# Kernel optimization log

Hardware: AMD Instinct MI355X
Metric: run time of the kernel (lower is better)

Reference implementation:

```python
import jax, jax.numpy as jnp
import numpy as np

# Layered-DAG regularization of the dynamic active_path graph.
H, N, BATCH, D, R = 6, 16, 32, 512, 64   # hop levels, nodes/level, batch, dim, low-rank
M = (H - 1) * N                           # nodes with weights (levels 1..H-1)
ETA_W = 0.015
LAM_C, LAM_R = 0.65, 0.35
THETA0 = 0.5
SPEC_MIN, SPEC_MAX = 0.3, 4.0
BETA1, BETA2, EPS = 0.9, 0.999, 1e-8
W_MAX = float(np.sqrt(D) * 2.0)
DW_CLIP = 5.0


def _spectral_norm(A1, B1):
    # largest singular value of W = A1 @ B1.T via power iteration using only low-rank products
    d = A1.shape[0]
    def body(_, u):
        w = A1 @ (B1.T @ (B1 @ (A1.T @ u)))  # (W W^T) u
        return w / (jnp.linalg.norm(w) + 1e-12)
    u0 = jnp.ones((d,), A1.dtype) / jnp.sqrt(jnp.asarray(d, A1.dtype))
    u = jax.lax.fori_loop(0, 20, body, u0)
    return jnp.linalg.norm(B1 @ (A1.T @ u))


def _update_node(A1, B1, mA, vA, mB, vB, Vin, T_local):
    # dual-signal (contrastive + retrograde) weight update, Adam step t=1, is_positive=True
    W = A1 @ B1.T                       # (D, D)
    Vw = Vin @ W.T                      # (BATCH, D) pre-activation (record.V_weighted)
    Vout = jnp.tanh(Vw)                 # record.V_out (tanh primitive)
    fprime = 1.0 - Vout ** 2            # primitive_derivative for tanh
    goodness = (Vout ** 2).sum(-1).mean()
    theta = THETA0 * ((Vin ** 2).sum(-1).mean() + 1e-9)   # goodness_scale_input=True
    delta = goodness - theta
    Vout_grad = (Vout * fprime * delta).mean(0)
    Vin_mean = Vin.mean(0)
    dW_c = jnp.outer(Vout_grad, Vin_mean)
    dW_r = jnp.outer(T_local.mean(0) * fprime.mean(0), Vin_mean)
    dW = LAM_C * dW_c + LAM_R * dW_r
    gnorm = jnp.linalg.norm(dW)
    dW = dW * jnp.where(gnorm > DW_CLIP, DW_CLIP / (gnorm + 1e-12), 1.0)
    gA = dW @ B1
    gB = dW.T @ A1
    mA_n = BETA1 * mA + (1 - BETA1) * gA
    vA_n = BETA2 * vA + (1 - BETA2) * gA ** 2
    A_new = A1 - ETA_W * (mA_n / (1 - BETA1)) / (jnp.sqrt(vA_n / (1 - BETA2)) + EPS)
    mB_n = BETA1 * mB + (1 - BETA1) * gB
    vB_n = BETA2 * vB + (1 - BETA2) * gB ** 2
    B_new = B1 - ETA_W * (mB_n / (1 - BETA1)) / (jnp.sqrt(vB_n / (1 - BETA2)) + EPS)
    return jnp.clip(A_new, -W_MAX, W_MAX), jnp.clip(B_new, -W_MAX, W_MAX)


def _forward(Y_hat, Y_star, V_edges, A, Bw, m_A, v_A, m_B, v_B):
    T_v = (Y_star - Y_hat) / jnp.sqrt(jnp.asarray(D, Y_hat.dtype))
    mse = jnp.mean((Y_star - Y_hat) ** 2)

    # proportional blame: per-edge mean-over-batch L2 norm of the contribution
    norms = jnp.linalg.norm(V_edges, axis=-1).mean(-1)           # (H-1, Ndst, Nsrc)
    w_blame = norms / (norms.sum(-1, keepdims=True) + 1e-9)

    spec = jax.vmap(jax.vmap(_spectral_norm))(A, Bw)             # (H-1, N)
    scale = jax.lax.stop_gradient(jnp.clip(spec, SPEC_MIN, SPEC_MAX))  # torch.tensor() detaches

    # retrograde flow in reverse topological (hop) order; output node = (level H-1, node 0)
    T_top = jnp.zeros((N, BATCH, D), Y_hat.dtype).at[0].set(T_v)

    def step(T_curr, xs):
        w_h, s_h = xs                                            # (Ndst,Nsrc), (Ndst,)
        tnorm = jnp.linalg.norm(T_curr, axis=-1).mean(-1)        # (Ndst,)
        edge_t = s_h[:, None] * w_h * tnorm[:, None]             # ||T_upstream|| per edge
        T_prev = jnp.einsum('j,ji,jbd->ibd', s_h, w_h, T_curr)   # blame-weighted scatter
        return T_prev, (T_prev, edge_t)

    _, (Ts, edge_t) = jax.lax.scan(step, T_top, (w_blame[::-1], scale[::-1]))
    T_all = jnp.concatenate([Ts[::-1], T_top[None]], axis=0)     # (H, N, BATCH, D), by level
    edge_tensions = edge_t[::-1]                                 # (H-1, Ndst, Nsrc)

    V_in = V_edges.sum(axis=2)                                   # inbox sum -> (H-1, N, BATCH, D)
    T_upd = T_all[1:]                                            # tensions at non-input nodes

    sh = (M, D, R)
    A_new, B_new = jax.vmap(_update_node)(
        A.reshape(sh), Bw.reshape(sh), m_A.reshape(sh), v_A.reshape(sh),
        m_B.reshape(sh), v_B.reshape(sh),
        V_in.reshape(M, BATCH, D), T_upd.reshape(M, BATCH, D))
    return (mse, edge_tensions,
            A_new.reshape(H - 1, N, D, R), B_new.reshape(H - 1, N, D, R), T_all)


def setup_inputs():
    key = jax.random.key(0)
    k = jax.random.split(key, 7)
    sd = 1.0 / np.sqrt(D)
    return {
        "Y_hat": jax.random.normal(k[0], (BATCH, D), jnp.float32),
        "Y_star": jax.random.normal(k[1], (BATCH, D), jnp.float32),
        "V_edges": jax.random.normal(k[2], (H - 1, N, N, BATCH, D), jnp.float32),
        "A": jax.random.normal(k[3], (H - 1, N, D, R), jnp.float32) * sd,
        "Bw": jax.random.normal(k[4], (H - 1, N, D, R), jnp.float32) * sd,
        "m_A": jnp.zeros((H - 1, N, D, R), jnp.float32),
        "v_A": jax.random.uniform(k[5], (H - 1, N, D, R), jnp.float32) * 1e-4,
        "m_B": jnp.zeros((H - 1, N, D, R), jnp.float32),
        "v_B": jax.random.uniform(k[6], (H - 1, N, D, R), jnp.float32) * 1e-4,
    }


def reference(Y_hat, Y_star, V_edges, A, Bw, m_A, v_A, m_B, v_B):
    return _forward(Y_hat, Y_star, V_edges, A, Bw, m_A, v_A, m_B, v_B)
```

## Files before the change

kernel.cpp:

```cpp
#include <hip/hip_runtime.h>
#include <math.h>

#define DEV static __device__ __forceinline__

constexpr int NB    = 16;
constexpr int BATCH = 32;
constexpr int DDIM  = 512;
constexpr int RK    = 64;
constexpr int LAY   = 5;
constexpr int MM    = 80;
constexpr int TLS   = NB * BATCH * DDIM;

constexpr float ETA_W   = 0.015f;
constexpr float LAM_C   = 0.65f, LAM_R = 0.35f;
constexpr float THETA0  = 0.5f;
constexpr float SPEC_MIN = 0.3f, SPEC_MAX = 4.0f;
constexpr float DW_CLIP = 5.0f;
constexpr float W_MAX   = 45.254833995939045f;
constexpr float RSQ_D   = 0.044194173824159216f;

constexpr int OUT_MSE  = 0;
constexpr int OUT_EDGE = 1;
constexpr int OUT_A    = 1281;
constexpr int OUT_B    = OUT_A + MM * DDIM * RK;
constexpr int OUT_T    = OUT_B + MM * DDIM * RK;

constexpr int SCR_VIN  = 2622724;

constexpr int WS_NORMB  = 0;
constexpr int WS_TVN    = 40960;
constexpr int WS_TVM    = 41000;
constexpr int WS_COEF   = 41600;
constexpr int WS_SCALE  = 41700;
constexpr int WS_VM     = 42000;
constexpr int WS_P      = 83000;
constexpr int WS_Q      = 88200;
constexpr int WS_GC     = 93400;

DEV float wave_reduce(float v) {
  #pragma unroll
  for (int o = 32; o > 0; o >>= 1) v += __shfl_down(v, o, 64);
  return v;
}

DEV float block_reduce_512(float v, float* sred) {
  v = wave_reduce(v);
  __syncthreads();
  if ((threadIdx.x & 63) == 0) sred[threadIdx.x >> 6] = v;
  __syncthreads();
  float s = 0.f;
  #pragma unroll
  for (int k = 0; k < 8; ++k) s += sred[k];
  return s;
}

DEV float bcast_lane(float v, int lane) {
  return __int_as_float(__builtin_amdgcn_readlane(__float_as_int(v), lane));
}

__global__ __launch_bounds__(256) void k_stage1(const float* __restrict__ V,
    const float* __restrict__ yh, const float* __restrict__ ys,
    float* __restrict__ out, float* __restrict__ ws) {
  __shared__ float sbuf[16][256];
  int bid = blockIdx.x, t = threadIdx.x;
  if (bid < 2560) {
    int b = bid & 31, j = (bid >> 5) & 15, hh = bid >> 9;
    const float* base = V + (size_t)(((hh*16 + j)*16)*32 + b) * 512;
    float ax = 0.f, ay = 0.f;
    #pragma unroll
    for (int i = 0; i < 16; ++i) {
      float2 vv = ((const float2*)(base + (size_t)i * 16384))[t];
      sbuf[i][t] = vv.x*vv.x + vv.y*vv.y;
      ax += vv.x; ay += vv.y;
    }
    float2 o; o.x = ax; o.y = ay;
    ((float2*)(out + SCR_VIN + (size_t)((hh*16 + j)*32 + b) * 512))[t] = o;
    __syncthreads();
    int w = t >> 6, lane = t & 63;
    #pragma unroll
    for (int k = 0; k < 4; ++k) {
      int i = w * 4 + k;
      float s = sbuf[i][lane] + sbuf[i][lane+64] + sbuf[i][lane+128] + sbuf[i][lane+192];
      s = wave_reduce(s);
      if (lane == 0)
        ws[WS_NORMB + (size_t)((hh*16 + j)*16 + i) * 32 + b] = sqrtf(s);
    }
  } else if (bid < 2592) {
    int b = bid - 2560;
    float2 a = ((const float2*)(yh + (size_t)b * 512))[t];
    float2 c = ((const float2*)(ys + (size_t)b * 512))[t];
    float d0 = c.x - a.x, d1 = c.y - a.y;
    float s = d0*d0 + d1*d1;
    s = wave_reduce(s);
    if ((t & 63) == 0) sbuf[0][t >> 6] = s;
    __syncthreads();
    if (t == 0)
      ws[WS_TVN + b] = sqrtf(sbuf[0][0]+sbuf[0][1]+sbuf[0][2]+sbuf[0][3]) * RSQ_D;
  } else if (bid == 2592) {
    float s = 0.f;
    for (int i = t; i < 4096; i += 256) {
      float4 a = ((const float4*)yh)[i], b = ((const float4*)ys)[i];
      float d0 = b.x-a.x, d1 = b.y-a.y, d2 = b.z-a.z, d3 = b.w-a.w;
      s += d0*d0 + d1*d1 + d2*d2 + d3*d3;
    }
    s = wave_reduce(s);
    if ((t & 63) == 0) sbuf[0][t >> 6] = s;
    __syncthreads();
    if (t == 0)
      out[OUT_MSE] = (sbuf[0][0]+sbuf[0][1]+sbuf[0][2]+sbuf[0][3]) * (1.f/16384.f);
  } else {
    float s0 = 0.f, s1 = 0.f;
    #pragma unroll 4
    for (int b = 0; b < 32; ++b) {
      s0 += ys[b*512 + t]       - yh[b*512 + t];
      s1 += ys[b*512 + t + 256] - yh[b*512 + t + 256];
    }
    ws[WS_TVM + t]       = s0 * (RSQ_D / 32.f);
    ws[WS_TVM + t + 256] = s1 * (RSQ_D / 32.f);
  }
}

__global__ __launch_bounds__(256) void k_gp(const float* __restrict__ Aw,
                                            const float* __restrict__ Bww,
                                            float* __restrict__ ws) {
  __shared__ float tile[128 * 64];
  __shared__ float GH[2][4096];
  __shared__ float y0s[4][64];
  int m = blockIdx.x;
  int t = threadIdx.x;
  int r1 = (t >> 4) * 4, r2 = (t & 15) * 4;
  const float* A1 = Aw  + (size_t)m * 32768;
  const float* B1 = Bww + (size_t)m * 32768;
  float acc[4][4];
  float y0acc = 0.f;

  #pragma unroll
  for (int i = 0; i < 4; ++i)
    #pragma unroll
    for (int k = 0; k < 4; ++k) acc[i][k] = 0.f;
  for (int slice = 0; slice < 4; ++slice) {
    __syncthreads();
    const float* src = A1 + slice * 8192;
    #pragma unroll
    for (int k = 0; k < 8; ++k)
      ((float4*)tile)[t + k * 256] = ((const float4*)src)[t + k * 256];
    __syncthreads();
    {
      int rr = t & 63, q = t >> 6;
      float s = 0.f;
      #pragma unroll 8
      for (int dd = q*32; dd < q*32 + 32; ++dd) s += tile[dd*64 + rr];
      y0s[q][rr] = s;
    }
    __syncthreads();
    if (t < 64) y0acc += y0s[0][t] + y0s[1][t] + y0s[2][t] + y0s[3][t];
    #pragma unroll 4
    for (int dd = 0; dd < 128; ++dd) {
      float4 a1 = *(const float4*)&tile[dd*64 + r1];
      float4 a2 = *(const float4*)&tile[dd*64 + r2];
      float av[4] = {a1.x, a1.y, a1.z, a1.w};
      float bv[4] = {a2.x, a2.y, a2.z, a2.w};
      #pragma unroll
      for (int i = 0; i < 4; ++i)
        #pragma unroll
        for (int k = 0; k < 4; ++k) acc[i][k] += av[i] * bv[k];
    }
  }
  #pragma unroll
  for (int i = 0; i < 4; ++i)
    #pragma unroll
    for (int k = 0; k < 4; ++k) GH[0][(r1+i)*64 + r2+k] = acc[i][k];

  #pragma unroll
  for (int i = 0; i < 4; ++i)
    #pragma unroll
    for (int k = 0; k < 4; ++k) acc[i][k] = 0.f;
  for (int slice = 0; slice < 4; ++slice) {
    __syncthreads();
    const float* src = B1 + slice * 8192;
    #pragma unroll
    for (int k = 0; k < 8; ++k)
      ((float4*)tile)[t + k * 256] = ((const float4*)src)[t + k * 256];
    __syncthreads();
    #pragma unroll 4
    for (int dd = 0; dd < 128; ++dd) {
      float4 a1 = *(const float4*)&tile[dd*64 + r1];
      float4 a2 = *(const float4*)&tile[dd*64 + r2];
      float av[4] = {a1.x, a1.y, a1.z, a1.w};
      float bv[4] = {a2.x, a2.y, a2.z, a2.w};
      #pragma unroll
      for (int i = 0; i < 4; ++i)
        #pragma unroll
        for (int k = 0; k < 4; ++k) acc[i][k] += av[i] * bv[k];
    }
  }
  #pragma unroll
  for (int i = 0; i < 4; ++i)
    #pragma unroll
    for (int k = 0; k < 4; ++k) GH[1][(r1+i)*64 + r2+k] = acc[i][k];
  __syncthreads();

  if (t < 64) {
    int r = t;
    float y = y0acc * RSQ_D;
    for (int it = 0; it < 20; ++it) {
      float z0=0.f, z1=0.f, z2=0.f, z3=0.f;
      #pragma unroll
      for (int c = 0; c < 16; ++c) {
        z0 = fmaf(GH[1][ c      *64 + r], bcast_lane(y, c),      z0);
        z1 = fmaf(GH[1][(c+16)*64 + r], bcast_lane(y, c+16),   z1);
        z2 = fmaf(GH[1][(c+32)*64 + r], bcast_lane(y, c+32),   z2);
        z3 = fmaf(GH[1][(c+48)*64 + r], bcast_lane(y, c+48),   z3);
      }
      float z = (z0+z1) + (z2+z3);
      float t0=0.f, t1=0.f, t2=0.f, t3=0.f;
      #pragma unroll
      for (int c = 0; c < 16; ++c) {
        t0 = fmaf(GH[0][ c      *64 + r], bcast_lane(z, c),      t0);
        t1 = fmaf(GH[0][(c+16)*64 + r], bcast_lane(z, c+16),   t1);
        t2 = fmaf(GH[0][(c+32)*64 + r], bcast_lane(z, c+32),   t2);
        t3 = fmaf(GH[0][(c+48)*64 + r], bcast_lane(z, c+48),   t3);
      }
      float tt = (t0+t1) + (t2+t3);
      float zt = z * tt;
      #pragma unroll
      for (int o = 32; o > 0; o >>= 1) zt += __shfl_xor(zt, o, 64);
      y = tt / (sqrtf(zt) + 1e-12f);
    }
    float z0=0.f, z1=0.f, z2=0.f, z3=0.f;
    #pragma unroll
    for (int c = 0; c < 16; ++c) {
      z0 = fmaf(GH[1][ c      *64 + r], bcast_lane(y, c),      z0);
      z1 = fmaf(GH[1][(c+16)*64 + r], bcast_lane(y, c+16),   z1);
      z2 = fmaf(GH[1][(c+32)*64 + r], bcast_lane(y, c+32),   z2);
      z3 = fmaf(GH[1][(c+48)*64 + r], bcast_lane(y, c+48),   z3);
    }
    float z = (z0+z1) + (z2+z3);
    float yz = y * z;
    #pragma unroll
    for (int o = 32; o > 0; o >>= 1) yz += __shfl_xor(yz, o, 64);
    if (r == 0)
      ws[WS_SCALE + m] = fminf(fmaxf(sqrtf(yz), SPEC_MIN), SPEC_MAX);
  }
}

__global__ __launch_bounds__(256) void k_cc(float* __restrict__ ws,
                                            float* __restrict__ out) {
  __shared__ float C[5 * 256];
  __shared__ float coef[6 * 16];
  int t = threadIdx.x;
  int j = t >> 4;
  #pragma unroll
  for (int h = 0; h < 5; ++h) {
    const float* nb = ws + WS_NORMB + (size_t)(h * 256 + t) * 32;
    float n = 0.f;
    #pragma unroll 8
    for (int b = 0; b < 32; ++b) n += nb[b];
    n *= (1.f / 32.f);
    float s = n;
    s += __shfl_xor(s, 1, 64);
    s += __shfl_xor(s, 2, 64);
    s += __shfl_xor(s, 4, 64);
    s += __shfl_xor(s, 8, 64);
    C[h * 256 + t] = ws[WS_SCALE + h * 16 + j] * n / (s + 1e-9f);
  }
  if (t < 16) coef[5 * 16 + t] = (t == 0) ? 1.f : 0.f;
  __syncthreads();
  if (t < 16) {
    for (int h = 4; h >= 0; --h) {
      float s = 0.f;
      #pragma unroll
      for (int jj = 0; jj < 16; ++jj)
        s += C[h * 256 + jj * 16 + t] * coef[(h + 1) * 16 + jj];
      coef[h * 16 + t] = s;
    }
  }
  __syncthreads();
  float tvs = 0.f;
  #pragma unroll
  for (int b = 0; b < 32; ++b) tvs += ws[WS_TVN + b];
  float tvmean = tvs * (1.f / 32.f);
  #pragma unroll
  for (int h = 0; h < 5; ++h)
    out[OUT_EDGE + h * 256 + t] = C[h * 256 + t] * coef[(h + 1) * 16 + j] * tvmean;
  if (t < 96) ws[WS_COEF + t] = coef[t];
}

constexpr int MTP = 516;
constexpr int YVP = 36;

__global__ __launch_bounds__(512) void k_node(const float* __restrict__ Aw,
    const float* __restrict__ Bww, const float* out_all, float* __restrict__ ws) {
  __shared__ float MT[64 * MTP];
  __shared__ float R2[4096];
  __shared__ float gcol[512];
  __shared__ float sred[8];
  int m = blockIdx.x;
  int t = threadIdx.x;
  const float* A1  = Aw  + (size_t)m * 32768;
  const float* B1  = Bww + (size_t)m * 32768;
  const float* Vin = out_all + SCR_VIN + (size_t)m * 16384;
  int hh = m >> 4, j = m & 15;
  float coefval = ws[WS_COEF + (hh + 1) * 16 + j];

  auto stageT = [&](const float* src) {
    #pragma unroll
    for (int ch = 0; ch < 16; ++ch) {
      int g = ch * 2048 + t * 4;
      int d = g >> 6, r = g & 63;
      float4 v = *(const float4*)(src + g);
      MT[(r+0)*MTP + d] = v.x;
      MT[(r+1)*MTP + d] = v.y;
      MT[(r+2)*MTP + d] = v.z;
      MT[(r+3)*MTP + d] = v.w;
    }
  };

  stageT(B1);
  __syncthreads();

  {
    int rl = t & 31, bq = t >> 5;
    int b0 = bq * 2;
    float a00 = 0.f, a01 = 0.f, a10 = 0.f, a11 = 0.f;
    const float4* vp0 = (const float4*)(Vin + (size_t)b0 * 512);
    const float4* vp1 = (const float4*)(Vin + (size_t)(b0 + 1) * 512);
    #pragma unroll 4
    for (int d4 = 0; d4 < 128; ++d4) {
      float4 m0 = *(const float4*)&MT[rl * MTP + d4 * 4];
      float4 m1 = *(const float4*)&MT[(rl + 32) * MTP + d4 * 4];
      float4 v0 = vp0[d4];
      float4 v1 = vp1[d4];
      a00 += m0.x*v0.x + m0.y*v0.y + m0.z*v0.z + m0.w*v0.w;
      a01 += m0.x*v1.x + m0.y*v1.y + m0.z*v1.z + m0.w*v1.w;
      a10 += m1.x*v0.x + m1.y*v0.y + m1.z*v0.z + m1.w*v0.w;
      a11 += m1.x*v1.x + m1.y*v1.y + m1.z*v1.z + m1.w*v1.w;
    }
    R2[rl * YVP + b0]            = a00;
    R2[rl * YVP + b0 + 1]        = a01;
    R2[(rl + 32) * YVP + b0]     = a10;
    R2[(rl + 32) * YVP + b0 + 1] = a11;
  }
  __syncthreads();
  if (t < 64) {
    float s = 0.f;
    #pragma unroll 8
    for (int b = 0; b < 32; ++b) s += R2[t * YVP + b];
    ws[WS_P + m * 64 + t] = s * (1.f / 32.f);
  }
  float tmean, ssin, ssvm;
  {
    int d = t;
    float sv = 0.f, sq = 0.f;
    #pragma unroll 4
    for (int b = 0; b < 32; ++b) {
      float v = Vin[b * 512 + d];
      sv += v; sq += v * v;
    }
    float vmean = sv * (1.f / 32.f);
    tmean = coefval * ws[WS_TVM + d];
    ws[WS_VM + m * 512 + d] = vmean;
    ssin = block_reduce_512(sq, sred) * (1.f / 32.f);
    ssvm = block_reduce_512(vmean * vmean, sred);
  }
  __syncthreads();
  stageT(A1);
  __syncthreads();
  float gs = 0.f;
  float vga[4] = {0.f, 0.f, 0.f, 0.f}, fpa[4] = {0.f, 0.f, 0.f, 0.f};
  {
    int d4 = t >> 2, bg = t & 3;
    float acc[4][8];
    #pragma unroll
    for (int i = 0; i < 4; ++i)
      #pragma unroll
      for (int k = 0; k < 8; ++k) acc[i][k] = 0.f;
    #pragma unroll 2
    for (int rr = 0; rr < 64; ++rr) {
      float4 at = *(const float4*)&MT[rr * MTP + d4 * 4];
      float4 ya = *(const float4*)&R2[rr * YVP + bg * 8];
      float4 yb = *(const float4*)&R2[rr * YVP + bg * 8 + 4];
      float av[4] = {at.x, at.y, at.z, at.w};
      float yv[8] = {ya.x, ya.y, ya.z, ya.w, yb.x, yb.y, yb.z, yb.w};
      #pragma unroll
      for (int i = 0; i < 4; ++i)
        #pragma unroll
        for (int k = 0; k < 8; ++k) acc[i][k] += av[i] * yv[k];
    }
    #pragma unroll
    for (int i = 0; i < 4; ++i)
      #pragma unroll
      for (int k = 0; k < 8; ++k) {
        float vw = acc[i][k];
        float x = fminf(fmaxf(vw * 2.f, -40.f), 40.f);
        float e = __expf(x);
        float vo = (e - 1.f) / (e + 1.f);
        float fp = 1.f - vo * vo;
        gs += vo * vo;
        vga[i] += vo * fp;
        fpa[i] += fp;
      }
  }
  __syncthreads();
  {
    int d4 = t >> 2, bg = t & 3;
    #pragma unroll
    for (int i = 0; i < 4; ++i) {
      R2[bg * 512 + d4 * 4 + i] = vga[i];
      R2[2048 + bg * 512 + d4 * 4 + i] = fpa[i];
    }
  }
  float goodness = block_reduce_512(gs, sred) * (1.f / 32.f);
  float delta = goodness - THETA0 * (ssin + 1e-9f);
  {
    int d = t;
    float vg = R2[d] + R2[512 + d] + R2[1024 + d] + R2[1536 + d];
    float fp = R2[2048 + d] + R2[2048 + 512 + d] + R2[2048 + 1024 + d] + R2[2048 + 1536 + d];
    float g = LAM_C * delta * vg * (1.f / 32.f) + LAM_R * tmean * (fp * (1.f / 32.f));
    float gn2 = block_reduce_512(g * g, sred);
    float gnorm = sqrtf(gn2) * sqrtf(ssvm);
    float clipf = gnorm > DW_CLIP ? DW_CLIP / (gnorm + 1e-12f) : 1.f;
    float gcv = g * clipf;
    ws[WS_GC + m * 512 + d] = gcv;
    gcol[d] = gcv;
  }
  __syncthreads();
  {
    int r = t & 63, dq = t >> 6;
    float s = 0.f;
    #pragma unroll
    for (int k = 0; k < 16; ++k) {
      int d = dq * 64 + k * 4;
      float4 at = *(const float4*)&MT[r * MTP + d];
      float4 gv = *(const float4*)&gcol[d];
      s += at.x*gv.x + at.y*gv.y + at.z*gv.z + at.w*gv.w;
    }
    R2[dq * 64 + r] = s;
  }
  __syncthreads();
  if (t < 64) {
    float s = 0.f;
    #pragma unroll
    for (int p8 = 0; p8 < 8; ++p8) s += R2[p8 * 64 + t];
    ws[WS_Q + m * 64 + t] = s;
  }
}

constexpr int TW_BLOCKS = 1536;
constexpr int AD_HALF4  = 655360;

__global__ __launch_bounds__(256) void k_final(const float* __restrict__ yh,
    const float* __restrict__ ys,
    const float* __restrict__ Aw, const float* __restrict__ Bww,
    const float* __restrict__ mA, const float* __restrict__ vA,
    const float* __restrict__ mB, const float* __restrict__ vB,
    const float* __restrict__ ws, float* __restrict__ out) {
  int bid = blockIdx.x, t = threadIdx.x;
  if (bid < TW_BLOCKS) {
    int g0 = (bid * 256 + t) * 4;
    int li = g0 >> 14;
    int bd = g0 & 16383;
    float4 a = *(const float4*)(yh + bd);
    float4 b = *(const float4*)(ys + bd);
    float cf = ws[WS_COEF + li] * RSQ_D;
    out[OUT_T + g0 + 0] = cf * (b.x - a.x);
    out[OUT_T + g0 + 1] = cf * (b.y - a.y);
    out[OUT_T + g0 + 2] = cf * (b.z - a.z);
    out[OUT_T + g0 + 3] = cf * (b.w - a.w);
    return;
  }
  int idx = (bid - TW_BLOCKS) * 256 + t;
  bool isB = idx >= AD_HALF4;
  int e = (isB ? idx - AD_HALF4 : idx) * 4;
  int m = e >> 15;
  int rem = e & 32767;
  int d = rem >> 6;
  int r = rem & 63;
  float4 g4;
  const float *w0, *m0, *v0;
  int obase;
  if (!isB) {
    float gc = ws[WS_GC + m * 512 + d];
    float4 p = *(const float4*)&ws[WS_P + m * 64 + r];
    g4.x = gc * p.x; g4.y = gc * p.y; g4.z = gc * p.z; g4.w = gc * p.w;
    w0 = Aw; m0 = mA; v0 = vA; obase = OUT_A;
  } else {
    float vm = ws[WS_VM + m * 512 + d];
    float4 q = *(const float4*)&ws[WS_Q + m * 64 + r];
    g4.x = vm * q.x; g4.y = vm * q.y; g4.z = vm * q.z; g4.w = vm * q.w;
    w0 = Bww; m0 = mB; v0 = vB; obase = OUT_B;
  }
  float4 a4 = *(const float4*)&w0[e];
  float4 mm4 = *(const float4*)&m0[e];
  float4 vv4 = *(const float4*)&v0[e];
  float ga[4] = {g4.x, g4.y, g4.z, g4.w};
  float aa[4] = {a4.x, a4.y, a4.z, a4.w};
  float ma[4] = {mm4.x, mm4.y, mm4.z, mm4.w};
  float va[4] = {vv4.x, vv4.y, vv4.z, vv4.w};
  #pragma unroll
  for (int i = 0; i < 4; ++i) {
    float g = ga[i];
    float mn = 0.9f * ma[i] + 0.1f * g;
    float vn = 0.999f * va[i] + 0.001f * g * g;
    float u = aa[i] - ETA_W * (mn * 10.f) / (sqrtf(vn * 1000.f) + 1e-8f);
    u = fminf(fmaxf(u, -W_MAX), W_MAX);
    out[obase + e + i] = u;
  }
}

extern "C" void kernel_launch(void* const* d_in, const int* in_sizes, int n_in,
                              void* d_out, int out_size, void* d_ws, size_t ws_size,
                              hipStream_t stream) {
  (void)in_sizes; (void)n_in; (void)out_size; (void)ws_size;
  const float* Yh = (const float*)d_in[0];
  const float* Ys = (const float*)d_in[1];
  const float* V  = (const float*)d_in[2];
  const float* Aw = (const float*)d_in[3];
  const float* Bw = (const float*)d_in[4];
  const float* mA = (const float*)d_in[5];
  const float* vA = (const float*)d_in[6];
  const float* mB = (const float*)d_in[7];
  const float* vB = (const float*)d_in[8];
  float* out = (float*)d_out;
  float* ws  = (float*)d_ws;

  k_stage1<<<2594, 256, 0, stream>>>(V, Yh, Ys, out, ws);
  k_gp<<<80, 256, 0, stream>>>(Aw, Bw, ws);
  k_cc<<<1, 256, 0, stream>>>(ws, out);
  k_node<<<80, 512, 0, stream>>>(Aw, Bw, out, ws);
  k_final<<<TW_BLOCKS + 2 * (AD_HALF4 / 256), 256, 0, stream>>>(
      Yh, Ys, Aw, Bw, mA, vA, mB, vB, ws, out);
}
```

Measured before the change: 133.6 us.

## Split Gram computation across 640 blocks fused into stage1, separate power-iteration kernel

The per-node A^T A and B^T B Gram matrices were built serially by 80 blocks, four slices each. That work is now spread over 640 extra blocks inside the stage-1 kernel, which write partial Grams and partial column sums to scratch space in the output buffer. A new one-wave-per-node kernel sums the four partials into registers and runs the 20-step power iteration from registers instead of LDS. This exposes much more parallelism and overlaps Gram work with the V-edge reduction, at the cost of extra global scratch traffic and one more launch, and the register-resident 128-float arrays may spill.

```diff
diff --git a/kernel.cpp b/kernel.cpp
--- a/kernel.cpp
+++ b/kernel.cpp
@@ -25,17 +25,19 @@
 constexpr int OUT_B    = OUT_A + MM * DDIM * RK;
 constexpr int OUT_T    = OUT_B + MM * DDIM * RK;
 
-constexpr int SCR_VIN  = 2622724;
+constexpr int SCR_GP   = 1284;
+constexpr int SCR_VIN  = SCR_GP + 2621440;
 
 constexpr int WS_NORMB  = 0;
 constexpr int WS_TVN    = 40960;
 constexpr int WS_TVM    = 41000;
 constexpr int WS_COEF   = 41600;
 constexpr int WS_SCALE  = 41700;
-constexpr int WS_VM     = 42000;
-constexpr int WS_P      = 83000;
-constexpr int WS_Q      = 88200;
-constexpr int WS_GC     = 93400;
+constexpr int WS_Y0P    = 41800;
+constexpr int WS_VM     = 62300;
+constexpr int WS_P      = 103300;
+constexpr int WS_Q      = 108450;
+constexpr int WS_GC     = 113600;
 
 DEV float wave_reduce(float v) {
   #pragma unroll
@@ -60,10 +62,12 @@
 
 __global__ __launch_bounds__(256) void k_stage1(const float* __restrict__ V,
     const float* __restrict__ yh, const float* __restrict__ ys,
+    const float* __restrict__ Aw, const float* __restrict__ Bww,
     float* __restrict__ out, float* __restrict__ ws) {
-  __shared__ float sbuf[16][256];
+  __shared__ float smem[8448];
   int bid = blockIdx.x, t = threadIdx.x;
   if (bid < 2560) {
+    float (*sbuf)[256] = (float(*)[256])smem;
     int b = bid & 31, j = (bid >> 5) & 15, hh = bid >> 9;
     const float* base = V + (size_t)(((hh*16 + j)*16)*32 + b) * 512;
     float ax = 0.f, ay = 0.f;
@@ -92,10 +96,10 @@
     float d0 = c.x - a.x, d1 = c.y - a.y;
     float s = d0*d0 + d1*d1;
     s = wave_reduce(s);
-    if ((t & 63) == 0) sbuf[0][t >> 6] = s;
+    if ((t & 63) == 0) smem[t >> 6] = s;
     __syncthreads();
     if (t == 0)
-      ws[WS_TVN + b] = sqrtf(sbuf[0][0]+sbuf[0][1]+sbuf[0][2]+sbuf[0][3]) * RSQ_D;
+      ws[WS_TVN + b] = sqrtf(smem[0]+smem[1]+smem[2]+smem[3]) * RSQ_D;
   } else if (bid == 2592) {
     float s = 0.f;
     for (int i = t; i < 4096; i += 256) {
@@ -104,11 +108,11 @@
       s += d0*d0 + d1*d1 + d2*d2 + d3*d3;
     }
     s = wave_reduce(s);
-    if ((t & 63) == 0) sbuf[0][t >> 6] = s;
+    if ((t & 63) == 0) smem[t >> 6] = s;
     __syncthreads();
     if (t == 0)
-      out[OUT_MSE] = (sbuf[0][0]+sbuf[0][1]+sbuf[0][2]+sbuf[0][3]) * (1.f/16384.f);
-  } else {
+      out[OUT_MSE] = (smem[0]+smem[1]+smem[2]+smem[3]) * (1.f/16384.f);
+  } else if (bid == 2593) {
     float s0 = 0.f, s1 = 0.f;
     #pragma unroll 4
     for (int b = 0; b < 32; ++b) {
@@ -117,47 +121,36 @@
     }
     ws[WS_TVM + t]       = s0 * (RSQ_D / 32.f);
     ws[WS_TVM + t + 256] = s1 * (RSQ_D / 32.f);
-  }
-}
-
-__global__ __launch_bounds__(256) void k_gp(const float* __restrict__ Aw,
-                                            const float* __restrict__ Bww,
-                                            float* __restrict__ ws) {
-  __shared__ float tile[128 * 64];
-  __shared__ float GH[2][4096];
-  __shared__ float y0s[4][64];
-  int m = blockIdx.x;
-  int t = threadIdx.x;
-  int r1 = (t >> 4) * 4, r2 = (t & 15) * 4;
-  const float* A1 = Aw  + (size_t)m * 32768;
-  const float* B1 = Bww + (size_t)m * 32768;
-  float acc[4][4];
-  float y0acc = 0.f;
-
-  #pragma unroll
-  for (int i = 0; i < 4; ++i)
-    #pragma unroll
-    for (int k = 0; k < 4; ++k) acc[i][k] = 0.f;
-  for (int slice = 0; slice < 4; ++slice) {
-    __syncthreads();
-    const float* src = A1 + slice * 8192;
+  } else {
+    float* tile = smem;
+    float (*y0s)[64] = (float(*)[64])(smem + 8192);
+    int bid0 = bid - 2594;
+    int slice = bid0 & 3, side = (bid0 >> 2) & 1, m = bid0 >> 3;
+    const float* src = (side ? Bww : Aw) + (size_t)m * 32768 + slice * 8192;
     #pragma unroll
     for (int k = 0; k < 8; ++k)
       ((float4*)tile)[t + k * 256] = ((const float4*)src)[t + k * 256];
     __syncthreads();
     {
-      int rr = t & 63, q = t >> 6;
+      int r = t & 63, q = t >> 6;
       float s = 0.f;
       #pragma unroll 8
-      for (int dd = q*32; dd < q*32 + 32; ++dd) s += tile[dd*64 + rr];
-      y0s[q][rr] = s;
+      for (int dd = q * 32; dd < q * 32 + 32; ++dd) s += tile[dd * 64 + r];
+      y0s[q][r] = s;
     }
     __syncthreads();
-    if (t < 64) y0acc += y0s[0][t] + y0s[1][t] + y0s[2][t] + y0s[3][t];
+    if (side == 0 && t < 64)
+      ws[WS_Y0P + (m * 4 + slice) * 64 + t] = y0s[0][t] + y0s[1][t] + y0s[2][t] + y0s[3][t];
+    float acc[4][4];
+    #pragma unroll
+    for (int i = 0; i < 4; ++i)
+      #pragma unroll
+      for (int k = 0; k < 4; ++k) acc[i][k] = 0.f;
+    int r1 = (t >> 4) * 4, r2 = (t & 15) * 4;
     #pragma unroll 4
     for (int dd = 0; dd < 128; ++dd) {
-      float4 a1 = *(const float4*)&tile[dd*64 + r1];
-      float4 a2 = *(const float4*)&tile[dd*64 + r2];
+      float4 a1 = *(const float4*)&tile[dd * 64 + r1];
+      float4 a2 = *(const float4*)&tile[dd * 64 + r2];
       float av[4] = {a1.x, a1.y, a1.z, a1.w};
       float bv[4] = {a2.x, a2.y, a2.z, a2.w};
       #pragma unroll
@@ -165,83 +158,83 @@
         #pragma unroll
         for (int k = 0; k < 4; ++k) acc[i][k] += av[i] * bv[k];
     }
-  }
-  #pragma unroll
-  for (int i = 0; i < 4; ++i)
-    #pragma unroll
-    for (int k = 0; k < 4; ++k) GH[0][(r1+i)*64 + r2+k] = acc[i][k];
-
-  #pragma unroll
-  for (int i = 0; i < 4; ++i)
-    #pragma unroll
-    for (int k = 0; k < 4; ++k) acc[i][k] = 0.f;
-  for (int slice = 0; slice < 4; ++slice) {
-    __syncthreads();
-    const float* src = B1 + slice * 8192;
-    #pragma unroll
-    for (int k = 0; k < 8; ++k)
-      ((float4*)tile)[t + k * 256] = ((const float4*)src)[t + k * 256];
-    __syncthreads();
-    #pragma unroll 4
-    for (int dd = 0; dd < 128; ++dd) {
-      float4 a1 = *(const float4*)&tile[dd*64 + r1];
-      float4 a2 = *(const float4*)&tile[dd*64 + r2];
-      float av[4] = {a1.x, a1.y, a1.z, a1.w};
-      float bv[4] = {a2.x, a2.y, a2.z, a2.w};
-      #pragma unroll
-      for (int i = 0; i < 4; ++i)
-        #pragma unroll
-        for (int k = 0; k < 4; ++k) acc[i][k] += av[i] * bv[k];
-    }
-  }
-  #pragma unroll
-  for (int i = 0; i < 4; ++i)
-    #pragma unroll
-    for (int k = 0; k < 4; ++k) GH[1][(r1+i)*64 + r2+k] = acc[i][k];
-  __syncthreads();
-
-  if (t < 64) {
-    int r = t;
-    float y = y0acc * RSQ_D;
-    for (int it = 0; it < 20; ++it) {
-      float z0=0.f, z1=0.f, z2=0.f, z3=0.f;
-      #pragma unroll
-      for (int c = 0; c < 16; ++c) {
-        z0 = fmaf(GH[1][ c      *64 + r], bcast_lane(y, c),      z0);
-        z1 = fmaf(GH[1][(c+16)*64 + r], bcast_lane(y, c+16),   z1);
-        z2 = fmaf(GH[1][(c+32)*64 + r], bcast_lane(y, c+32),   z2);
-        z3 = fmaf(GH[1][(c+48)*64 + r], bcast_lane(y, c+48),   z3);
-      }
-      float z = (z0+z1) + (z2+z3);
-      float t0=0.f, t1=0.f, t2=0.f, t3=0.f;
-      #pragma unroll
-      for (int c = 0; c < 16; ++c) {
-        t0 = fmaf(GH[0][ c      *64 + r], bcast_lane(z, c),      t0);
-        t1 = fmaf(GH[0][(c+16)*64 + r], bcast_lane(z, c+16),   t1);
-        t2 = fmaf(GH[0][(c+32)*64 + r], bcast_lane(z, c+32),   t2);
-        t3 = fmaf(GH[0][(c+48)*64 + r], bcast_lane(z, c+48),   t3);
-      }
-      float tt = (t0+t1) + (t2+t3);
-      float zt = z * tt;
-      #pragma unroll
-      for (int o = 32; o > 0; o >>= 1) zt += __shfl_xor(zt, o, 64);
-      y = tt / (sqrtf(zt) + 1e-12f);
-    }
-    float z0=0.f, z1=0.f, z2=0.f, z3=0.f;
+    float* outp = out + SCR_GP + (size_t)((m * 2 + side) * 4 + slice) * 4096;
+    #pragma unroll
+    for (int i = 0; i < 4; ++i) {
+      float4 v; v.x = acc[i][0]; v.y = acc[i][1]; v.z = acc[i][2]; v.w = acc[i][3];
+      *(float4*)&outp[(r1 + i) * 64 + r2] = v;
+    }
+  }
+}
+
+__global__ __launch_bounds__(64, 1) void k_power(const float* __restrict__ out,
+                                                 float* __restrict__ ws) {
+  int m = blockIdx.x;
+  int r = threadIdx.x;
+  const float* gp = out + SCR_GP + (size_t)(m * 2 + 0) * 16384;
+  const float* hp = out + SCR_GP + (size_t)(m * 2 + 1) * 16384;
+  float Gc[64], Hc[64];
+  #pragma unroll
+  for (int c4 = 0; c4 < 16; ++c4) {
+    const float* gb = gp + r * 64 + c4 * 4;
+    float4 g0 = *(const float4*)(gb);
+    float4 g1 = *(const float4*)(gb + 4096);
+    float4 g2 = *(const float4*)(gb + 8192);
+    float4 g3 = *(const float4*)(gb + 12288);
+    Gc[c4*4+0] = g0.x+g1.x+g2.x+g3.x;
+    Gc[c4*4+1] = g0.y+g1.y+g2.y+g3.y;
+    Gc[c4*4+2] = g0.z+g1.z+g2.z+g3.z;
+    Gc[c4*4+3] = g0.w+g1.w+g2.w+g3.w;
+    const float* hb = hp + r * 64 + c4 * 4;
+    float4 h0 = *(const float4*)(hb);
+    float4 h1 = *(const float4*)(hb + 4096);
+    float4 h2 = *(const float4*)(hb + 8192);
+    float4 h3 = *(const float4*)(hb + 12288);
+    Hc[c4*4+0] = h0.x+h1.x+h2.x+h3.x;
+    Hc[c4*4+1] = h0.y+h1.y+h2.y+h3.y;
+    Hc[c4*4+2] = h0.z+h1.z+h2.z+h3.z;
+    Hc[c4*4+3] = h0.w+h1.w+h2.w+h3.w;
+  }
+  float y = (ws[WS_Y0P + (m*4+0)*64 + r] + ws[WS_Y0P + (m*4+1)*64 + r] +
+             ws[WS_Y0P + (m*4+2)*64 + r] + ws[WS_Y0P + (m*4+3)*64 + r]) * RSQ_D;
+  for (int it = 0; it < 20; ++it) {
+    float z0 = 0.f, z1 = 0.f, z2 = 0.f, z3 = 0.f;
     #pragma unroll
     for (int c = 0; c < 16; ++c) {
-      z0 = fmaf(GH[1][ c      *64 + r], bcast_lane(y, c),      z0);
-      z1 = fmaf(GH[1][(c+16)*64 + r], bcast_lane(y, c+16),   z1);
-      z2 = fmaf(GH[1][(c+32)*64 + r], bcast_lane(y, c+32),   z2);
-      z3 = fmaf(GH[1][(c+48)*64 + r], bcast_lane(y, c+48),   z3);
-    }
-    float z = (z0+z1) + (z2+z3);
-    float yz = y * z;
-    #pragma unroll
-    for (int o = 32; o > 0; o >>= 1) yz += __shfl_xor(yz, o, 64);
-    if (r == 0)
-      ws[WS_SCALE + m] = fminf(fmaxf(sqrtf(yz), SPEC_MIN), SPEC_MAX);
-  }
+      z0 = fmaf(Hc[c],      bcast_lane(y, c),      z0);
+      z1 = fmaf(Hc[c + 16], bcast_lane(y, c + 16), z1);
+      z2 = fmaf(Hc[c + 32], bcast_lane(y, c + 32), z2);
+      z3 = fmaf(Hc[c + 48], bcast_lane(y, c + 48), z3);
+    }
+    float z = (z0 + z1) + (z2 + z3);
+    float t0 = 0.f, t1 = 0.f, t2 = 0.f, t3 = 0.f;
+    #pragma unroll
+    for (int c = 0; c < 16; ++c) {
+      t0 = fmaf(Gc[c],      bcast_lane(z, c),      t0);
+      t1 = fmaf(Gc[c + 16], bcast_lane(z, c + 16), t1);
+      t2 = fmaf(Gc[c + 32], bcast_lane(z, c + 32), t2);
+      t3 = fmaf(Gc[c + 48], bcast_lane(z, c + 48), t3);
+    }
+    float tt = (t0 + t1) + (t2 + t3);
+    float zt = z * tt;
+    #pragma unroll
+    for (int o = 32; o > 0; o >>= 1) zt += __shfl_xor(zt, o, 64);
+    y = tt / (sqrtf(zt) + 1e-12f);
+  }
+  float z0 = 0.f, z1 = 0.f, z2 = 0.f, z3 = 0.f;
+  #pragma unroll
+  for (int c = 0; c < 16; ++c) {
+    z0 = fmaf(Hc[c],      bcast_lane(y, c),      z0);
+    z1 = fmaf(Hc[c + 16], bcast_lane(y, c + 16), z1);
+    z2 = fmaf(Hc[c + 32], bcast_lane(y, c + 32), z2);
+    z3 = fmaf(Hc[c + 48], bcast_lane(y, c + 48), z3);
+  }
+  float z = (z0 + z1) + (z2 + z3);
+  float yz = y * z;
+  #pragma unroll
+  for (int o = 32; o > 0; o >>= 1) yz += __shfl_xor(yz, o, 64);
+  if (r == 0)
+    ws[WS_SCALE + m] = fminf(fmaxf(sqrtf(yz), SPEC_MIN), SPEC_MAX);
 }
 
 __global__ __launch_bounds__(256) void k_cc(float* __restrict__ ws,
@@ -524,8 +517,8 @@
   float* out = (float*)d_out;
   float* ws  = (float*)d_ws;
 
-  k_stage1<<<2594, 256, 0, stream>>>(V, Yh, Ys, out, ws);
-  k_gp<<<80, 256, 0, stream>>>(Aw, Bw, ws);
+  k_stage1<<<2594 + 640, 256, 0, stream>>>(V, Yh, Ys, Aw, Bw, out, ws);
+  k_power<<<80, 64, 0, stream>>>(out, ws);
   k_cc<<<1, 256, 0, stream>>>(ws, out);
   k_node<<<80, 512, 0, stream>>>(Aw, Bw, out, ws);
   k_final<<<TW_BLOCKS + 2 * (AD_HALF4 / 256), 256, 0, stream>>>(
```

New measurement: 115.1 us. 1.16x faster.
